# Optimization experiments

Measured on AMD Instinct MI355X. Metric: run time of the kernel, lower is better.

## Reference

```python
import jax, jax.numpy as jnp
import numpy as np

N_NODES = 50000
EPS = 1e-5


def _gcn_edges(edge_index, num_nodes):
    # Add self loops (PyG GCNConv default) and compute symmetric normalization.
    src = jnp.concatenate([edge_index[0], jnp.arange(num_nodes, dtype=edge_index.dtype)])
    dst = jnp.concatenate([edge_index[1], jnp.arange(num_nodes, dtype=edge_index.dtype)])
    deg = jax.ops.segment_sum(jnp.ones_like(dst, dtype=jnp.float32), dst, num_segments=num_nodes)
    dinv = jnp.where(deg > 0, jax.lax.rsqrt(deg), 0.0)
    norm = dinv[src] * dinv[dst]  # [E+N]
    return src, dst, norm


def gcn_conv(x, W, b, src, dst, norm, num_nodes):
    xw = x @ W  # [N, out]
    msg = xw[src] * norm[:, None]  # [E+N, out] gather + scale
    out = jax.ops.segment_sum(msg, dst, num_segments=num_nodes)  # scatter-add
    return out + b


def layer_norm(x, g, b):
    mu = jnp.mean(x, axis=-1, keepdims=True)
    var = jnp.mean(jnp.square(x - mu), axis=-1, keepdims=True)
    return (x - mu) * jax.lax.rsqrt(var + EPS) * g + b


def setup_inputs() -> dict:
    key = jax.random.key(0)
    ks = jax.random.split(key, 12)
    d_in, d_h, d_out = 128, 128, 64
    n_edges = 800000
    x = jax.random.normal(ks[0], (N_NODES, d_in), dtype=jnp.float32)
    edge_index = jax.random.randint(ks[1], (2, n_edges), 0, N_NODES, dtype=jnp.int64)
    s = 1.0 / np.sqrt(d_in)
    return {
        "x": x,
        "edge_index": edge_index,
        "W1": jax.random.uniform(ks[2], (d_in, d_h), jnp.float32, -s, s),
        "b1": jnp.zeros((d_h,), jnp.float32),
        "W2": jax.random.uniform(ks[3], (d_h, d_h), jnp.float32, -s, s),
        "b2": jnp.zeros((d_h,), jnp.float32),
        "W3": jax.random.uniform(ks[4], (d_h, d_out), jnp.float32, -s, s),
        "b3": jnp.zeros((d_out,), jnp.float32),
        "g1": jnp.ones((d_h,), jnp.float32),
        "be1": jnp.zeros((d_h,), jnp.float32),
        "g2": jnp.ones((d_h,), jnp.float32),
        "be2": jnp.zeros((d_h,), jnp.float32),
    }


def reference(x, edge_index, W1, b1, W2, b2, W3, b3, g1, be1, g2, be2):
    num_nodes = x.shape[0]
    src, dst, norm = _gcn_edges(edge_index, num_nodes)
    h = jax.nn.relu(gcn_conv(x, W1, b1, src, dst, norm, num_nodes))
    h = layer_norm(h, g1, be1)  # dropout is identity in eval mode
    h = jax.nn.relu(gcn_conv(h, W2, b2, src, dst, norm, num_nodes))
    h = layer_norm(h, g2, be2)
    return gcn_conv(h, W3, b3, src, dst, norm, num_nodes)
```

## Files before the change

### kernel.cpp

```cpp
#include <hip/hip_runtime.h>

#define EPSV 1e-5f

typedef _Float16 half2_t __attribute__((ext_vector_type(2)));
typedef _Float16 half8_t __attribute__((ext_vector_type(8)));
typedef float float4_t __attribute__((ext_vector_type(4)));

#define BINSH 6
#define BINSZ 64


__global__ __launch_bounds__(256) void k_init(
    const float* __restrict__ W1, const float* __restrict__ W2,
    const float* __restrict__ W3, _Float16* __restrict__ Wh1,
    _Float16* __restrict__ Wh2, _Float16* __restrict__ Wh3,
    const int* __restrict__ src, const int* __restrict__ dst,
    int* __restrict__ cursor, int* __restrict__ csr, int E, int N) {
  int bid = blockIdx.x;
  if (bid < 20) {
    const float* W;
    _Float16* Wh;
    int COLS, t;
    if (bid < 8) { W = W1; Wh = Wh1; COLS = 128; t = bid * 256 + threadIdx.x; }
    else if (bid < 16) { W = W2; Wh = Wh2; COLS = 128; t = (bid - 8) * 256 + threadIdx.x; }
    else { W = W3; Wh = Wh3; COLS = 64; t = (bid - 16) * 256 + threadIdx.x; }
    int NT = (COLS / 16) * 4 * 64;
    if (t >= NT) return;
    int lane = t & 63;
    int ks = (t >> 6) & 3;
    int nb = t >> 8;
    int col = nb * 16 + (lane & 15);
    int k0 = ks * 32 + (lane >> 4) * 8;
    half8_t v;
#pragma unroll
    for (int j = 0; j < 8; j++) v[j] = (_Float16)W[(size_t)(k0 + j) * COLS + col];
    *(half8_t*)&Wh[(size_t)t * 8] = v;
    return;
  }
  int b = bid - 20;
  int slice = b & 7;
  int lo = (int)(((long long)N * slice) >> 3);
  int hi = (int)(((long long)N * (slice + 1)) >> 3);
  int r = (b >> 3) * 256 + threadIdx.x;
  int stride = (4096 >> 3) * 256;
  for (int e = r; e < E; e += stride) {
    int d = __builtin_nontemporal_load(&dst[e]);
    if (d >= lo && d < hi) {
      int s = __builtin_nontemporal_load(&src[e]);
      int pos = atomicAdd(&cursor[d], 1);
      if (pos < BINSZ) csr[((size_t)d << BINSH) + pos] = s;
    }
  }
}


template <int COLS, bool LN, typename AT>
__device__ __forceinline__ void gemm_body(
    int bx, const AT* __restrict__ A, const float2* __restrict__ lnp,
    const float* __restrict__ g, const float* __restrict__ be,
    const _Float16* __restrict__ Wh, const int* __restrict__ cursor,
    _Float16* __restrict__ out, int N, int N1) {
  constexpr int NB = COLS / 16;
  int lane = threadIdx.x & 63;
  int w = threadIdx.x >> 6;
  int quad = lane >> 4;
  int mrow = bx * 64 + w * 16 + (lane & 15);
  half8_t af[4];
  if (mrow < N) {
    if constexpr (LN) {
      float P = 0.f, Q = 0.f;
#pragma unroll
      for (int s = 0; s < 4; s++) {
        float2 pq = lnp[(size_t)s * N + mrow];
        P += pq.x; Q += pq.y;
      }
      float mean = P * (1.f / 128.f);
      float rstd = rsqrtf(Q * (1.f / 128.f) - mean * mean + EPSV);
#pragma unroll
      for (int ks = 0; ks < 4; ks++) {
        half8_t sv = *(const half8_t*)&A[((size_t)ks * N1 + mrow) * 32 + quad * 8];
        float4 g0 = *(const float4*)&g[ks * 32 + quad * 8];
        float4 g1 = *(const float4*)&g[ks * 32 + quad * 8 + 4];
        float4 e0 = *(const float4*)&be[ks * 32 + quad * 8];
        float4 e1 = *(const float4*)&be[ks * 32 + quad * 8 + 4];
        af[ks][0] = (_Float16)fmaf(((float)sv[0] - mean) * rstd, g0.x, e0.x);
        af[ks][1] = (_Float16)fmaf(((float)sv[1] - mean) * rstd, g0.y, e0.y);
        af[ks][2] = (_Float16)fmaf(((float)sv[2] - mean) * rstd, g0.z, e0.z);
        af[ks][3] = (_Float16)fmaf(((float)sv[3] - mean) * rstd, g0.w, e0.w);
        af[ks][4] = (_Float16)fmaf(((float)sv[4] - mean) * rstd, g1.x, e1.x);
        af[ks][5] = (_Float16)fmaf(((float)sv[5] - mean) * rstd, g1.y, e1.y);
        af[ks][6] = (_Float16)fmaf(((float)sv[6] - mean) * rstd, g1.z, e1.z);
        af[ks][7] = (_Float16)fmaf(((float)sv[7] - mean) * rstd, g1.w, e1.w);
      }
    } else {
      const AT* ap = A + (size_t)mrow * 128 + quad * 8;
#pragma unroll
      for (int ks = 0; ks < 4; ks++) {
        float4 f0 = *(const float4*)(ap + ks * 32);
        float4 f1 = *(const float4*)(ap + ks * 32 + 4);
        af[ks][0] = (_Float16)f0.x; af[ks][1] = (_Float16)f0.y;
        af[ks][2] = (_Float16)f0.z; af[ks][3] = (_Float16)f0.w;
        af[ks][4] = (_Float16)f1.x; af[ks][5] = (_Float16)f1.y;
        af[ks][6] = (_Float16)f1.z; af[ks][7] = (_Float16)f1.w;
      }
    }
  } else {
#pragma unroll
    for (int ks = 0; ks < 4; ks++)
#pragma unroll
      for (int j = 0; j < 8; j++) af[ks][j] = (_Float16)0.f;
  }
  float4_t acc[NB];
#pragma unroll
  for (int nb = 0; nb < NB; nb++) acc[nb] = (float4_t){0.f, 0.f, 0.f, 0.f};
#pragma unroll
  for (int nb = 0; nb < NB; nb++) {
#pragma unroll
    for (int ks = 0; ks < 4; ks++) {
      half8_t bf = *(const half8_t*)&Wh[(size_t)((nb * 4 + ks) * 64 + lane) * 8];
      acc[nb] = __builtin_amdgcn_mfma_f32_16x16x32_f16(af[ks], bf, acc[nb], 0, 0, 0);
    }
  }
  int orow0 = bx * 64 + w * 16 + quad * 4;
#pragma unroll
  for (int r = 0; r < 4; r++) {
    int row = orow0 + r;
    if (row < N) {
      float dv = rsqrtf((float)(min(cursor[row], BINSZ) + 1));
#pragma unroll
      for (int nb = 0; nb < NB; nb++) {
        int dim = nb * 16 + (lane & 15);
        out[((size_t)(dim >> 5) * N1 + row) * 32 + (dim & 31)] =
            (_Float16)(acc[nb][r] * dv);
      }
    }
  }
}


__global__ __launch_bounds__(256) void k_gemm1_prep(
    const float* __restrict__ x, const _Float16* __restrict__ Wh1,
    const int* __restrict__ cursor, int* __restrict__ csr,
    _Float16* __restrict__ ys_y, _Float16* __restrict__ ys3,
    int N, int N1, int gb) {
  if ((int)blockIdx.x < gb) {
    gemm_body<128, false, float>(blockIdx.x, x, nullptr, nullptr, nullptr, Wh1,
                                 cursor, ys_y, N, N1);
    return;
  }
  int i = (blockIdx.x - gb) * 256 + threadIdx.x;
  if (i < N) {
    int cnt = min(cursor[i], BINSZ);
    int cr = (cnt + 15) & ~15;
    for (int p = cnt; p < cr; p++) csr[((size_t)i << BINSH) + p] = N;
  }
  if (i < 64) {
    ((half2_t*)ys_y)[((size_t)(i >> 4) * N1 + N) * 16 + (i & 15)] = (half2_t){0, 0};
  } else if (i < 96) {
    int j = i - 64;
    ((half2_t*)ys3)[((size_t)(j >> 4) * N1 + N) * 16 + (j & 15)] = (half2_t){0, 0};
  }
}

template <int COLS, bool LN, typename AT>
__global__ __launch_bounds__(256) void k_gemm_mfma(
    const AT* __restrict__ A, const float2* __restrict__ lnp,
    const float* __restrict__ g, const float* __restrict__ be,
    const _Float16* __restrict__ Wh, const int* __restrict__ cursor,
    _Float16* __restrict__ out, int N, int N1) {
  gemm_body<COLS, LN, AT>(blockIdx.x, A, lnp, g, be, Wh, cursor, out, N, N1);
}


__global__ __launch_bounds__(256) void k_aggs(
    const _Float16* __restrict__ ysrc, const int* __restrict__ csr,
    const int* __restrict__ cursor, const float* __restrict__ b,
    _Float16* __restrict__ sdst, float2* __restrict__ lnp, int N, int N1) {
  int slice = blockIdx.x & 3;
  int lane = threadIdx.x & 63;
  int g = lane >> 4, li = lane & 15;
  int q = li & 3, es = li >> 2;
  int node = (blockIdx.x >> 2) * 16 + (threadIdx.x >> 6) * 4 + g;
  const half8_t* yb = (const half8_t*)ysrc + (size_t)slice * N1 * 4;
  int cnt = 0;
  if (node < N) cnt = min(cursor[node], BINSZ);
  int cround = (cnt + 15) & ~15;
  size_t bin = (size_t)node << BINSH;
  float acc[8];
#pragma unroll
  for (int j = 0; j < 8; j++) acc[j] = 0.f;
  const half2_t one2 = {(_Float16)1.f, (_Float16)1.f};
  for (int c = 0; c < cround; c += 16) {
    int idx = csr[bin + c + li];
#pragma unroll
    for (int p = 0; p < 2; p++) {
      int sa = __shfl(idx, (g << 4) | (es << 2) | (p << 1), 64);
      int sb = __shfl(idx, (g << 4) | (es << 2) | (p << 1) | 1, 64);
      half8_t ua = yb[(size_t)sa * 4 + q];
      half8_t ub = yb[(size_t)sb * 4 + q];
      const unsigned int* wa = (const unsigned int*)&ua;
      const unsigned int* wb = (const unsigned int*)&ub;
#pragma unroll
      for (int w = 0; w < 4; w++) {
        unsigned int p0 = __builtin_amdgcn_perm(wa[w], wb[w], 0x01000504u);
        unsigned int p1 = __builtin_amdgcn_perm(wa[w], wb[w], 0x03020706u);
        acc[2 * w] = __builtin_amdgcn_fdot2(
            __builtin_bit_cast(half2_t, p0), one2, acc[2 * w], false);
        acc[2 * w + 1] = __builtin_amdgcn_fdot2(
            __builtin_bit_cast(half2_t, p1), one2, acc[2 * w + 1], false);
      }
    }
  }
#pragma unroll
  for (int j = 0; j < 8; j++) {
    acc[j] += __shfl_xor(acc[j], 4, 64);
    acc[j] += __shfl_xor(acc[j], 8, 64);
  }
  half8_t us = yb[(size_t)min(node, N) * 4 + q];
#pragma unroll
  for (int j = 0; j < 8; j++) acc[j] += (float)us[j];
  float di = rsqrtf((float)(cnt + 1));
  float4 b0 = ((const float4*)b)[slice * 8 + q * 2];
  float4 b1 = ((const float4*)b)[slice * 8 + q * 2 + 1];
  float v[8];
  v[0] = fmaxf(fmaf(acc[0], di, b0.x), 0.f);
  v[1] = fmaxf(fmaf(acc[1], di, b0.y), 0.f);
  v[2] = fmaxf(fmaf(acc[2], di, b0.z), 0.f);
  v[3] = fmaxf(fmaf(acc[3], di, b0.w), 0.f);
  v[4] = fmaxf(fmaf(acc[4], di, b1.x), 0.f);
  v[5] = fmaxf(fmaf(acc[5], di, b1.y), 0.f);
  v[6] = fmaxf(fmaf(acc[6], di, b1.z), 0.f);
  v[7] = fmaxf(fmaf(acc[7], di, b1.w), 0.f);
  float p = 0.f, qs = 0.f;
#pragma unroll
  for (int j = 0; j < 8; j++) {
    p += v[j];
    qs = fmaf(v[j], v[j], qs);
  }
  p += __shfl_xor(p, 1, 64);
  p += __shfl_xor(p, 2, 64);
  qs += __shfl_xor(qs, 1, 64);
  qs += __shfl_xor(qs, 2, 64);
  if (node < N) {
    if (li == 0) lnp[(size_t)slice * N + node] = make_float2(p, qs);
    if (es == 0) {
      half8_t o;
#pragma unroll
      for (int j = 0; j < 8; j++) o[j] = (_Float16)v[j];
      ((half8_t*)sdst)[((size_t)slice * N1 + node) * 4 + q] = o;
    }
  }
}


__global__ __launch_bounds__(256) void k_agg_out(
    const _Float16* __restrict__ ysrc, const int* __restrict__ csr,
    const int* __restrict__ cursor, const float* __restrict__ b,
    float* __restrict__ out, int N, int N1) {
  int slice = blockIdx.x & 1;
  int lane = threadIdx.x & 63;
  int g = lane >> 4, li = lane & 15;
  int q = li & 3, es = li >> 2;
  int node = (blockIdx.x >> 1) * 16 + (threadIdx.x >> 6) * 4 + g;
  const half8_t* yb = (const half8_t*)ysrc + (size_t)slice * N1 * 4;
  int cnt = 0;
  if (node < N) cnt = min(cursor[node], BINSZ);
  int cround = (cnt + 15) & ~15;
  size_t bin = (size_t)node << BINSH;
  float acc[8];
#pragma unroll
  for (int j = 0; j < 8; j++) acc[j] = 0.f;
  const half2_t one2 = {(_Float16)1.f, (_Float16)1.f};
  for (int c = 0; c < cround; c += 16) {
    int idx = csr[bin + c + li];
#pragma unroll
    for (int p = 0; p < 2; p++) {
      int sa = __shfl(idx, (g << 4) | (es << 2) | (p << 1), 64);
      int sb = __shfl(idx, (g << 4) | (es << 2) | (p << 1) | 1, 64);
      half8_t ua = yb[(size_t)sa * 4 + q];
      half8_t ub = yb[(size_t)sb * 4 + q];
      const unsigned int* wa = (const unsigned int*)&ua;
      const unsigned int* wb = (const unsigned int*)&ub;
#pragma unroll
      for (int w = 0; w < 4; w++) {
        unsigned int p0 = __builtin_amdgcn_perm(wa[w], wb[w], 0x01000504u);
        unsigned int p1 = __builtin_amdgcn_perm(wa[w], wb[w], 0x03020706u);
        acc[2 * w] = __builtin_amdgcn_fdot2(
            __builtin_bit_cast(half2_t, p0), one2, acc[2 * w], false);
        acc[2 * w + 1] = __builtin_amdgcn_fdot2(
            __builtin_bit_cast(half2_t, p1), one2, acc[2 * w + 1], false);
      }
    }
  }
#pragma unroll
  for (int j = 0; j < 8; j++) {
    acc[j] += __shfl_xor(acc[j], 4, 64);
    acc[j] += __shfl_xor(acc[j], 8, 64);
  }
  if (node < N && es == 0) {
    half8_t us = yb[(size_t)node * 4 + q];
#pragma unroll
    for (int j = 0; j < 8; j++) acc[j] += (float)us[j];
    float di = rsqrtf((float)(cnt + 1));
    float4 b0 = ((const float4*)b)[slice * 8 + q * 2];
    float4 b1 = ((const float4*)b)[slice * 8 + q * 2 + 1];
    float4 o0, o1;
    o0.x = fmaf(acc[0], di, b0.x);
    o0.y = fmaf(acc[1], di, b0.y);
    o0.z = fmaf(acc[2], di, b0.z);
    o0.w = fmaf(acc[3], di, b0.w);
    o1.x = fmaf(acc[4], di, b1.x);
    o1.y = fmaf(acc[5], di, b1.y);
    o1.z = fmaf(acc[6], di, b1.z);
    o1.w = fmaf(acc[7], di, b1.w);
    ((float4*)out)[(size_t)node * 16 + slice * 8 + q * 2] = o0;
    ((float4*)out)[(size_t)node * 16 + slice * 8 + q * 2 + 1] = o1;
  }
}


extern "C" void kernel_launch(void* const* d_in, const int* in_sizes, int n_in,
                              void* d_out, int out_size, void* d_ws, size_t ws_size,
                              hipStream_t stream) {
  const float* x = (const float*)d_in[0];
  const int* ei = (const int*)d_in[1];
  const float* W1 = (const float*)d_in[2];
  const float* b1 = (const float*)d_in[3];
  const float* W2 = (const float*)d_in[4];
  const float* b2 = (const float*)d_in[5];
  const float* W3 = (const float*)d_in[6];
  const float* b3 = (const float*)d_in[7];
  const float* g1 = (const float*)d_in[8];
  const float* be1 = (const float*)d_in[9];
  const float* g2 = (const float*)d_in[10];
  const float* be2 = (const float*)d_in[11];

  int N = in_sizes[0] / 128;
  int E = in_sizes[1] / 2;
  int N1 = N + 1;
  const int* srcs = ei;
  const int* dsts = ei + E;

  char* ws = (char*)d_ws;
  size_t off = 0;
  auto alloc = [&](size_t bytes) -> char* {
    char* p = ws + off;
    off = (off + bytes + 255) & ~(size_t)255;
    return p;
  };
  int* cursor = (int*)alloc((size_t)N * 4);
  int* csr = (int*)alloc((size_t)N * BINSZ * 4);
  _Float16* ys_y = (_Float16*)alloc((size_t)4 * N1 * 32 * 2);
  _Float16* ys_s = (_Float16*)alloc((size_t)4 * N1 * 32 * 2);
  _Float16* ys3 = (_Float16*)alloc((size_t)2 * N1 * 32 * 2);
  float2* lnp = (float2*)alloc((size_t)4 * N * 8);
  _Float16* Wh1 = (_Float16*)alloc(128 * 128 * 2);
  _Float16* Wh2 = (_Float16*)alloc(128 * 128 * 2);
  _Float16* Wh3 = (_Float16*)alloc(128 * 64 * 2);

  int gb = (N + 63) / 64;
  int pb = (N + 255) / 256;
  int nb16 = (N + 15) / 16;

  hipMemsetAsync(cursor, 0, (size_t)N * sizeof(int), stream);
  k_init<<<4116, 256, 0, stream>>>(W1, W2, W3, Wh1, Wh2, Wh3,
                                   srcs, dsts, cursor, csr, E, N);
  k_gemm1_prep<<<gb + pb, 256, 0, stream>>>(x, Wh1, cursor, csr, ys_y, ys3,
                                            N, N1, gb);
  k_aggs<<<nb16 * 4, 256, 0, stream>>>(ys_y, csr, cursor, b1, ys_s, lnp, N, N1);
  k_gemm_mfma<128, true, _Float16><<<gb, 256, 0, stream>>>(
      ys_s, lnp, g1, be1, Wh2, cursor, ys_y, N, N1);
  k_aggs<<<nb16 * 4, 256, 0, stream>>>(ys_y, csr, cursor, b2, ys_s, lnp, N, N1);
  k_gemm_mfma<64, true, _Float16><<<gb, 256, 0, stream>>>(
      ys_s, lnp, g2, be2, Wh3, cursor, ys3, N, N1);
  k_agg_out<<<nb16 * 2, 256, 0, stream>>>(ys3, csr, cursor, b3,
                                          (float*)d_out, N, N1);
}
```

Before: 245.3 us.

## Split preprocessing, vectorize edge binning, mask CSR padding in aggregation

The cursor memset and the weight conversion move into a new k_pre kernel, which also zeroes the padding rows. The edge binning kernel now reads src and dst as int4 and handles four edges per iteration, loading src unconditionally. The CSR padding-fill pass is dropped; the aggregation kernels instead substitute index N for lanes past the real count. This removes the memset call and the separate padding writes but adds a kernel launch, and every slice now reads the src array in full.

```diff
diff --git a/kernel.cpp b/kernel.cpp
--- a/kernel.cpp
+++ b/kernel.cpp
@@ -10,12 +10,12 @@
 #define BINSZ 64
 
 
-__global__ __launch_bounds__(256) void k_init(
+__global__ __launch_bounds__(256) void k_pre(
     const float* __restrict__ W1, const float* __restrict__ W2,
     const float* __restrict__ W3, _Float16* __restrict__ Wh1,
     _Float16* __restrict__ Wh2, _Float16* __restrict__ Wh3,
-    const int* __restrict__ src, const int* __restrict__ dst,
-    int* __restrict__ cursor, int* __restrict__ csr, int E, int N) {
+    int* __restrict__ cursor, _Float16* __restrict__ ys_y,
+    _Float16* __restrict__ ys3, int N, int N1, int zb) {
   int bid = blockIdx.x;
   if (bid < 20) {
     const float* W;
@@ -37,18 +37,66 @@
     *(half8_t*)&Wh[(size_t)t * 8] = v;
     return;
   }
-  int b = bid - 20;
+  if (bid < 20 + zb) {
+    int i4 = (bid - 20) * 256 + threadIdx.x;
+    if (i4 < ((N + 3) >> 2)) ((int4*)cursor)[i4] = make_int4(0, 0, 0, 0);
+    return;
+  }
+  int t = threadIdx.x;
+  half8_t z;
+#pragma unroll
+  for (int j = 0; j < 8; j++) z[j] = (_Float16)0.f;
+  if (t < 16) {
+    int s = t >> 2, qq = t & 3;
+    *(half8_t*)&ys_y[((size_t)s * N1 + N) * 32 + qq * 8] = z;
+  } else if (t < 24) {
+    int j = t - 16;
+    int s = j >> 2, qq = j & 3;
+    *(half8_t*)&ys3[((size_t)s * N1 + N) * 32 + qq * 8] = z;
+  }
+}
+
+
+__global__ __launch_bounds__(256) void k_init(
+    const int* __restrict__ src, const int* __restrict__ dst,
+    int* __restrict__ cursor, int* __restrict__ csr, int E, int N) {
+  int b = blockIdx.x;
   int slice = b & 7;
   int lo = (int)(((long long)N * slice) >> 3);
   int hi = (int)(((long long)N * (slice + 1)) >> 3);
   int r = (b >> 3) * 256 + threadIdx.x;
-  int stride = (4096 >> 3) * 256;
-  for (int e = r; e < E; e += stride) {
-    int d = __builtin_nontemporal_load(&dst[e]);
-    if (d >= lo && d < hi) {
-      int s = __builtin_nontemporal_load(&src[e]);
-      int pos = atomicAdd(&cursor[d], 1);
-      if (pos < BINSZ) csr[((size_t)d << BINSH) + pos] = s;
+  const int stride = (4096 >> 3) * 256;
+  int E4 = E >> 2;
+  const int4* dst4 = (const int4*)dst;
+  const int4* src4 = (const int4*)src;
+  for (int e4 = r; e4 < E4; e4 += stride) {
+    int4 d4 = dst4[e4];
+    int4 s4 = src4[e4];
+    if (d4.x >= lo && d4.x < hi) {
+      int pos = atomicAdd(&cursor[d4.x], 1);
+      if (pos < BINSZ) csr[((size_t)d4.x << BINSH) + pos] = s4.x;
+    }
+    if (d4.y >= lo && d4.y < hi) {
+      int pos = atomicAdd(&cursor[d4.y], 1);
+      if (pos < BINSZ) csr[((size_t)d4.y << BINSH) + pos] = s4.y;
+    }
+    if (d4.z >= lo && d4.z < hi) {
+      int pos = atomicAdd(&cursor[d4.z], 1);
+      if (pos < BINSZ) csr[((size_t)d4.z << BINSH) + pos] = s4.z;
+    }
+    if (d4.w >= lo && d4.w < hi) {
+      int pos = atomicAdd(&cursor[d4.w], 1);
+      if (pos < BINSZ) csr[((size_t)d4.w << BINSH) + pos] = s4.w;
+    }
+  }
+  if ((E & 3) && (b >> 3) == 0) {
+    for (int e = (E & ~3) + threadIdx.x; e < E; e += 256) {
+      int d = dst[e];
+      if (d >= lo && d < hi) {
+        int s = src[e];
+        int pos = atomicAdd(&cursor[d], 1);
+        if (pos < BINSZ) csr[((size_t)d << BINSH) + pos] = s;
+      }
     }
   }
 }
@@ -137,31 +185,6 @@
   }
 }
 
-
-__global__ __launch_bounds__(256) void k_gemm1_prep(
-    const float* __restrict__ x, const _Float16* __restrict__ Wh1,
-    const int* __restrict__ cursor, int* __restrict__ csr,
-    _Float16* __restrict__ ys_y, _Float16* __restrict__ ys3,
-    int N, int N1, int gb) {
-  if ((int)blockIdx.x < gb) {
-    gemm_body<128, false, float>(blockIdx.x, x, nullptr, nullptr, nullptr, Wh1,
-                                 cursor, ys_y, N, N1);
-    return;
-  }
-  int i = (blockIdx.x - gb) * 256 + threadIdx.x;
-  if (i < N) {
-    int cnt = min(cursor[i], BINSZ);
-    int cr = (cnt + 15) & ~15;
-    for (int p = cnt; p < cr; p++) csr[((size_t)i << BINSH) + p] = N;
-  }
-  if (i < 64) {
-    ((half2_t*)ys_y)[((size_t)(i >> 4) * N1 + N) * 16 + (i & 15)] = (half2_t){0, 0};
-  } else if (i < 96) {
-    int j = i - 64;
-    ((half2_t*)ys3)[((size_t)(j >> 4) * N1 + N) * 16 + (j & 15)] = (half2_t){0, 0};
-  }
-}
-
 template <int COLS, bool LN, typename AT>
 __global__ __launch_bounds__(256) void k_gemm_mfma(
     const AT* __restrict__ A, const float2* __restrict__ lnp,
@@ -191,7 +214,8 @@
   for (int j = 0; j < 8; j++) acc[j] = 0.f;
   const half2_t one2 = {(_Float16)1.f, (_Float16)1.f};
   for (int c = 0; c < cround; c += 16) {
-    int idx = csr[bin + c + li];
+    int idx = N;
+    if (c + li < cnt) idx = csr[bin + c + li];
 #pragma unroll
     for (int p = 0; p < 2; p++) {
       int sa = __shfl(idx, (g << 4) | (es << 2) | (p << 1), 64);
@@ -272,7 +296,8 @@
   for (int j = 0; j < 8; j++) acc[j] = 0.f;
   const half2_t one2 = {(_Float16)1.f, (_Float16)1.f};
   for (int c = 0; c < cround; c += 16) {
-    int idx = csr[bin + c + li];
+    int idx = N;
+    if (c + li < cnt) idx = csr[bin + c + li];
 #pragma unroll
     for (int p = 0; p < 2; p++) {
       int sa = __shfl(idx, (g << 4) | (es << 2) | (p << 1), 64);
@@ -359,14 +384,14 @@
   _Float16* Wh3 = (_Float16*)alloc(128 * 64 * 2);
 
   int gb = (N + 63) / 64;
-  int pb = (N + 255) / 256;
   int nb16 = (N + 15) / 16;
-
-  hipMemsetAsync(cursor, 0, (size_t)N * sizeof(int), stream);
-  k_init<<<4116, 256, 0, stream>>>(W1, W2, W3, Wh1, Wh2, Wh3,
-                                   srcs, dsts, cursor, csr, E, N);
-  k_gemm1_prep<<<gb + pb, 256, 0, stream>>>(x, Wh1, cursor, csr, ys_y, ys3,
-                                            N, N1, gb);
+  int zb = (((N + 3) >> 2) + 255) >> 8;
+
+  k_pre<<<20 + zb + 1, 256, 0, stream>>>(W1, W2, W3, Wh1, Wh2, Wh3,
+                                         cursor, ys_y, ys3, N, N1, zb);
+  k_init<<<4096, 256, 0, stream>>>(srcs, dsts, cursor, csr, E, N);
+  k_gemm_mfma<128, false, float><<<gb, 256, 0, stream>>>(
+      x, nullptr, nullptr, nullptr, Wh1, cursor, ys_y, N, N1);
   k_aggs<<<nb16 * 4, 256, 0, stream>>>(ys_y, csr, cursor, b1, ys_s, lnp, N, N1);
   k_gemm_mfma<128, true, _Float16><<<gb, 256, 0, stream>>>(
       ys_s, lnp, g1, be1, Wh2, cursor, ys_y, N, N1);
```

Measured after the change: 244.2 us. No clear change (-0.4%).
